# Performance work log

Hardware: AMD Instinct MI355X
Metric: run time of the kernel (lower is better)

The kernel has to match this reference:

```python
import jax, jax.numpy as jnp
import numpy as np

B, S, H, Q = 32, 128, 128, 3  # users, seq_len, hidden_size, quadkey_level
L = Q - 1  # number of mixing scales


def setup_inputs() -> dict:
    key = jax.random.key(0)
    ks = jax.random.split(key, 12)
    trend0 = jax.random.normal(ks[0], (B, S, H), dtype=jnp.float32)
    trend1 = jax.random.normal(ks[1], (B, S, H), dtype=jnp.float32)
    trend2 = jax.random.normal(ks[2], (B, S, H), dtype=jnp.float32)
    # Per-position prefix linears padded into dense tensors, zero-masked beyond
    # the prefix length j+1 so the ragged math is exact:
    #   W1[j, :j+1, :j+1] ~ Linear(j+1, j+1), b1[j, :j+1]
    #   W2[j, :j+1]      ~ Linear(j+1, 1),   b2[j]
    idx = jnp.arange(S)
    pm = (idx[None, :] <= idx[:, None]).astype(jnp.float32)  # [j, s]: s <= j
    W1 = jax.random.normal(ks[3], (L, S, S, S), dtype=jnp.float32) * 0.05
    W1 = W1 * pm[None, :, :, None] * pm[None, :, None, :]
    b1 = jax.random.normal(ks[4], (L, S, S), dtype=jnp.float32) * 0.05 * pm[None]
    W2 = jax.random.normal(ks[5], (L, S, S), dtype=jnp.float32) * 0.05 * pm[None]
    b2 = jax.random.normal(ks[6], (L, S), dtype=jnp.float32) * 0.05
    # shared output MLP: Linear(H,H)->GELU->Linear(H,H); stored as [in, out]
    Wm1 = jax.random.normal(ks[7], (H, H), dtype=jnp.float32) * 0.05
    bm1 = jax.random.normal(ks[8], (H,), dtype=jnp.float32) * 0.05
    Wm2 = jax.random.normal(ks[9], (H, H), dtype=jnp.float32) * 0.05
    bm2 = jax.random.normal(ks[10], (H,), dtype=jnp.float32) * 0.05
    return {"trend0": trend0, "trend1": trend1, "trend2": trend2,
            "W1": W1, "b1": b1, "W2": W2, "b2": b2,
            "Wm1": Wm1, "bm1": bm1, "Wm2": Wm2, "bm2": bm2}


def reference(trend0, trend1, trend2, W1, b1, W2, b2, Wm1, bm1, Wm2, bm2):
    gelu = lambda x: jax.nn.gelu(x, approximate=False)  # torch nn.GELU default
    mlp = lambda x: gelu(x @ Wm1 + bm1) @ Wm2 + bm2

    rev = [trend2, trend1, trend0]  # trend_list reversed
    out_low = rev[0]
    out_high = rev[1]
    outs = [out_low]
    for i in range(Q - 1):
        # vectorized ragged prefix mix: per position j, out_low[:, :j+1] (as [B,H,j+1])
        # -> Linear(j+1,j+1) -> GELU -> Linear(j+1,1). Zero-padding in W1/b1/W2
        # kills all contributions beyond the prefix (GELU(0)=0).
        y1 = jnp.einsum('bsh,jst->bhjt', out_low, W1[i]) + b1[i]  # [B,H,S,S]
        res = jnp.einsum('bhjt,jt->bjh', gelu(y1), W2[i]) + b2[i][None, :, None]
        out_high = out_high + res
        out_low = out_high
        if i + 2 <= Q - 1:
            out_high = rev[i + 2]
        out_low = mlp(out_low)
        outs.append(out_low)
    outs.reverse()
    return tuple(outs)
```

## Files before the change

kernel.cpp:

```cpp
#include <hip/hip_runtime.h>
#include <stdint.h>

#define BSH (32 * 128 * 128)

typedef __attribute__((ext_vector_type(8))) __bf16 bf16x8;
typedef __attribute__((ext_vector_type(4))) float f32x4;

__device__ __forceinline__ unsigned short f2bf(float f) {
  union { float f; unsigned u; } v; v.f = f;
  return (unsigned short)((v.u + 0x7FFFu + ((v.u >> 16) & 1u)) >> 16);
}

__device__ __forceinline__ float fast_exp2(float x) {
#if __has_builtin(__builtin_amdgcn_exp2f)
  return __builtin_amdgcn_exp2f(x);
#else
  float r; asm("v_exp_f32 %0, %1" : "=v"(r) : "v"(x)); return r;
#endif
}
__device__ __forceinline__ float fast_rcp(float x) {
#if __has_builtin(__builtin_amdgcn_rcpf)
  return __builtin_amdgcn_rcpf(x);
#else
  float r; asm("v_rcp_f32 %0, %1" : "=v"(r) : "v"(x)); return r;
#endif
}

__device__ __forceinline__ float gelu_f(float y) {
  float u = y * y;
  float p = __builtin_fmaf(u, 0.044715f, 1.0f) * y;
  float w = fast_exp2(p * 2.30220787f);
  return y - y * fast_rcp(1.0f + w);
}

__device__ __forceinline__ void transpose_block_c(const float* __restrict__ src,
                                                  unsigned short* __restrict__ dst,
                                                  unsigned short* lds) {
  const int tid = threadIdx.x;
  const float4* s4 = (const float4*)(src);
#pragma unroll
  for (int it = 0; it < 16; ++it) {
    int i4 = tid + it * 256;
    float4 v = s4[i4];
    int s = i4 >> 5;
    int t0 = (i4 * 4) & 127;
    unsigned short* pp = lds + s * 136 + t0;
    pp[0] = f2bf(v.x); pp[1] = f2bf(v.y); pp[2] = f2bf(v.z); pp[3] = f2bf(v.w);
  }
  __syncthreads();
#pragma unroll
  for (int it = 0; it < 8; ++it) {
    int c = tid + it * 256;
    int sc = c >> 7, tr = c & 127;
    unsigned short tmp[8] __attribute__((aligned(16)));
#pragma unroll
    for (int e = 0; e < 8; ++e) tmp[e] = lds[(sc * 8 + e) * 136 + tr];
    *(uint4*)(dst + (sc * 128 + tr) * 8) = *(const uint4*)tmp;
  }
}

__global__ __launch_bounds__(256) void prepass_kernel(
    const float* __restrict__ W1, const float* __restrict__ trend2,
    const float* __restrict__ Wm1, const float* __restrict__ Wm2,
    unsigned short* __restrict__ W1Tc, unsigned short* __restrict__ T2c,
    unsigned short* __restrict__ Wm1c, unsigned short* __restrict__ Wm2c,
    float* __restrict__ out2) {
  __shared__ unsigned short lds[128 * 136];
  const int bid = blockIdx.x;
  if (bid < 256) {
    int x = bid & 7, i = bid >> 3;
    int stage = i >> 4, u = i & 15;
    int m = u & 7, half = u >> 3;
    int jpp = x + 8 * m;
    int j = half ? 127 - jpp : jpp;
    int blk = stage * 128 + j;
    transpose_block_c(W1 + blk * 16384, W1Tc + blk * 16384, lds);
  } else if (bid < 288) {
    const int b = bid - 256;
    transpose_block_c(trend2 + b * 16384, T2c + b * 16384, lds);
    const float4* s4 = (const float4*)(trend2 + b * 16384);
    float4* d4 = (float4*)(out2 + b * 16384);
#pragma unroll
    for (int it = 0; it < 16; ++it)
      d4[threadIdx.x + it * 256] = s4[threadIdx.x + it * 256];
  } else if (bid == 288) {
    transpose_block_c(Wm1, Wm1c, lds);
  } else {
    transpose_block_c(Wm2, Wm2c, lds);
  }
}

__global__ __launch_bounds__(256, 3) void mix_mlp_kernel(
    const unsigned short* __restrict__ XTc,
    const unsigned short* __restrict__ W1Tj,
    const float* __restrict__ b1j,
    const float* __restrict__ W2j,
    const float* __restrict__ b2j,
    const float* __restrict__ trendR,
    const unsigned short* __restrict__ Wm1c,
    const unsigned short* __restrict__ Wm2c,
    const float* __restrict__ bm1,
    const float* __restrict__ bm2,
    float* __restrict__ outA,
    unsigned short* __restrict__ outTc) {
  __shared__ float res[512];
  __shared__ __align__(16) float xrow[2][128];
  __shared__ __align__(16) unsigned short urow[2][128];
  const int bid = blockIdx.x;
  const int b = bid >> 6;
  const int jp = bid & 63;
  const int js = jp, jb = 127 - jp;
  const int tid = threadIdx.x;
  const int wave = tid >> 6;
  const int p = wave & 1;
  const int mh = wave >> 1;
  const int lane = tid & 63;
  const int lane15 = lane & 15;
  const int quad = lane >> 4;

  const int nt_s = (js >> 4) + 1, ks_s = (js >> 5) + 1;
  const int nt_b = (jb >> 4) + 1, ks_b = (jb >> 5) + 1;

  const unsigned short* Bp = XTc + b * 16384 + (p * 64 + lane15) * 8;
  const unsigned short* As = W1Tj + js * 16384 + lane15 * 8;
  const unsigned short* Ab = W1Tj + jb * 16384 + lane15 * 8;
  const float C = -2.45546937f;

  bf16x8 Bv[4][4];
#pragma unroll
  for (int ks = 0; ks < 4; ++ks)
    if (ks < ks_b) {
      const int ko = (ks * 4 + quad) * 1024;
      Bv[ks][0] = *(const bf16x8*)(Bp + ko);
      Bv[ks][1] = *(const bf16x8*)(Bp + ko + 128);
      Bv[ks][2] = *(const bf16x8*)(Bp + ko + 256);
      Bv[ks][3] = *(const bf16x8*)(Bp + ko + 384);
    }

  float psum[2][4];
#pragma unroll
  for (int jj = 0; jj < 2; ++jj)
#pragma unroll
    for (int ni = 0; ni < 4; ++ni) psum[jj][ni] = 0.f;

  for (int mt = mh; mt < nt_b; mt += 2) {
    f32x4 acc[4];
#pragma unroll
    for (int ni = 0; ni < 4; ++ni) { f32x4 z = {0.f, 0.f, 0.f, 0.f}; acc[ni] = z; }
    const int mo = mt * 128;
#pragma unroll
    for (int ks = 0; ks < 4; ++ks)
      if (ks < ks_b) {
        bf16x8 a = *(const bf16x8*)(Ab + (ks * 4 + quad) * 1024 + mo);
        acc[0] = __builtin_amdgcn_mfma_f32_16x16x32_bf16(a, Bv[ks][0], acc[0], 0, 0, 0);
        acc[1] = __builtin_amdgcn_mfma_f32_16x16x32_bf16(a, Bv[ks][1], acc[1], 0, 0, 0);
        acc[2] = __builtin_amdgcn_mfma_f32_16x16x32_bf16(a, Bv[ks][2], acc[2], 0, 0, 0);
        acc[3] = __builtin_amdgcn_mfma_f32_16x16x32_bf16(a, Bv[ks][3], acc[3], 0, 0, 0);
      }
    const int tb = mt * 16 + quad * 4;
    float4 b1v = *(const float4*)(b1j + jb * 128 + tb);
    float4 w2v = *(const float4*)(W2j + jb * 128 + tb);
#pragma unroll
    for (int r = 0; r < 4; ++r) {
      float b1r = ((const float*)&b1v)[r];
      float w2r = ((const float*)&w2v)[r];
      float cb = C * b1r;
      float bw = b1r * w2r;
#pragma unroll
      for (int ni = 0; ni < 4; ++ni) {
        float a = acc[ni][r];
        float m = __builtin_fmaf(a, C, cb);
        float e = fast_exp2(m);
        float rr2 = fast_rcp(1.0f + e);
        float yw = __builtin_fmaf(a, w2r, bw);
        psum[1][ni] = __builtin_fmaf(yw, rr2, psum[1][ni]);
      }
    }
  }

  for (int mt = mh; mt < nt_s; mt += 2) {
    f32x4 acc[4];
#pragma unroll
    for (int ni = 0; ni < 4; ++ni) { f32x4 z = {0.f, 0.f, 0.f, 0.f}; acc[ni] = z; }
    const int mo = mt * 128;
#pragma unroll
    for (int ks = 0; ks < 2; ++ks)
      if (ks < ks_s) {
        bf16x8 a = *(const bf16x8*)(As + (ks * 4 + quad) * 1024 + mo);
        acc[0] = __builtin_amdgcn_mfma_f32_16x16x32_bf16(a, Bv[ks][0], acc[0], 0, 0, 0);
        acc[1] = __builtin_amdgcn_mfma_f32_16x16x32_bf16(a, Bv[ks][1], acc[1], 0, 0, 0);
        acc[2] = __builtin_amdgcn_mfma_f32_16x16x32_bf16(a, Bv[ks][2], acc[2], 0, 0, 0);
        acc[3] = __builtin_amdgcn_mfma_f32_16x16x32_bf16(a, Bv[ks][3], acc[3], 0, 0, 0);
      }
    const int tb = mt * 16 + quad * 4;
    float4 b1v = *(const float4*)(b1j + js * 128 + tb);
    float4 w2v = *(const float4*)(W2j + js * 128 + tb);
#pragma unroll
    for (int r = 0; r < 4; ++r) {
      float b1r = ((const float*)&b1v)[r];
      float w2r = ((const float*)&w2v)[r];
      float cb = C * b1r;
      float bw = b1r * w2r;
#pragma unroll
      for (int ni = 0; ni < 4; ++ni) {
        float a = acc[ni][r];
        float m = __builtin_fmaf(a, C, cb);
        float e = fast_exp2(m);
        float rr2 = fast_rcp(1.0f + e);
        float yw = __builtin_fmaf(a, w2r, bw);
        psum[0][ni] = __builtin_fmaf(yw, rr2, psum[0][ni]);
      }
    }
  }

#pragma unroll
  for (int jj = 0; jj < 2; ++jj)
#pragma unroll
    for (int ni = 0; ni < 4; ++ni) {
      float v = psum[jj][ni];
      v += __shfl_xor(v, 16, 64);
      v += __shfl_xor(v, 32, 64);
      psum[jj][ni] = v;
    }

  if (quad == 0) {
#pragma unroll
    for (int jj = 0; jj < 2; ++jj)
#pragma unroll
      for (int ni = 0; ni < 4; ++ni)
        res[wave * 128 + jj * 64 + ni * 16 + lane15] = psum[jj][ni];
  }
  __syncthreads();
  {
    const int l = tid & 15;
    const int nni = (tid >> 4) & 3;
    const int jj = (tid >> 6) & 1;
    const int pp = tid >> 7;
    const int j = jj ? jb : js;
    const int h = pp * 64 + nni * 16 + l;
    float v = res[tid] + res[tid + 256] + b2j[j] +
              trendR[(b * 128 + j) * 128 + h];
    xrow[jj][h] = v;
  }
  __syncthreads();

  const int arow = lane15 & 1;
  bf16x8 af[4];
#pragma unroll
  for (int ks = 0; ks < 4; ++ks) {
    const f32x4* xp = (const f32x4*)&xrow[arow][(ks * 4 + quad) * 8];
    f32x4 v0 = xp[0], v1 = xp[1];
    unsigned short t[8] __attribute__((aligned(16)));
    t[0] = f2bf(v0[0]); t[1] = f2bf(v0[1]); t[2] = f2bf(v0[2]); t[3] = f2bf(v0[3]);
    t[4] = f2bf(v1[0]); t[5] = f2bf(v1[1]); t[6] = f2bf(v1[2]); t[7] = f2bf(v1[3]);
    af[ks] = *(const bf16x8*)t;
  }
  f32x4 acc1[2];
  { f32x4 z = {0.f, 0.f, 0.f, 0.f}; acc1[0] = z; acc1[1] = z; }
#pragma unroll
  for (int ks = 0; ks < 4; ++ks) {
    int kq = ks * 4 + quad;
    bf16x8 w0 = *(const bf16x8*)(Wm1c + (kq * 128 + wave * 32 + lane15) * 8);
    bf16x8 w1 = *(const bf16x8*)(Wm1c + (kq * 128 + wave * 32 + 16 + lane15) * 8);
    acc1[0] = __builtin_amdgcn_mfma_f32_16x16x32_bf16(af[ks], w0, acc1[0], 0, 0, 0);
    acc1[1] = __builtin_amdgcn_mfma_f32_16x16x32_bf16(af[ks], w1, acc1[1], 0, 0, 0);
  }
  if (quad == 0) {
#pragma unroll
    for (int ni2 = 0; ni2 < 2; ++ni2) {
      int n = wave * 32 + ni2 * 16 + lane15;
      float bv = bm1[n];
      urow[0][n] = f2bf(gelu_f(acc1[ni2][0] + bv));
      urow[1][n] = f2bf(gelu_f(acc1[ni2][1] + bv));
    }
  }
  __syncthreads();
  bf16x8 uf[4];
#pragma unroll
  for (int ks = 0; ks < 4; ++ks)
    uf[ks] = *(const bf16x8*)&urow[arow][(ks * 4 + quad) * 8];
  f32x4 acc2[2];
  { f32x4 z = {0.f, 0.f, 0.f, 0.f}; acc2[0] = z; acc2[1] = z; }
#pragma unroll
  for (int ks = 0; ks < 4; ++ks) {
    int kq = ks * 4 + quad;
    bf16x8 w0 = *(const bf16x8*)(Wm2c + (kq * 128 + wave * 32 + lane15) * 8);
    bf16x8 w1 = *(const bf16x8*)(Wm2c + (kq * 128 + wave * 32 + 16 + lane15) * 8);
    acc2[0] = __builtin_amdgcn_mfma_f32_16x16x32_bf16(uf[ks], w0, acc2[0], 0, 0, 0);
    acc2[1] = __builtin_amdgcn_mfma_f32_16x16x32_bf16(uf[ks], w1, acc2[1], 0, 0, 0);
  }
  if (quad == 0) {
#pragma unroll
    for (int ni2 = 0; ni2 < 2; ++ni2) {
      int n = wave * 32 + ni2 * 16 + lane15;
      float bv = bm2[n];
#pragma unroll
      for (int r = 0; r < 2; ++r) {
        int j = r ? jb : js;
        float v = acc2[ni2][r] + bv;
        outA[(b * 128 + j) * 128 + n] = v;
        if (outTc)
          outTc[b * 16384 + ((j >> 3) * 128 + n) * 8 + (j & 7)] = f2bf(v);
      }
    }
  }
}

extern "C" void kernel_launch(void* const* d_in, const int* in_sizes, int n_in,
                              void* d_out, int out_size, void* d_ws, size_t ws_size,
                              hipStream_t stream) {
  (void)in_sizes; (void)n_in; (void)out_size; (void)ws_size;
  const float* trend0 = (const float*)d_in[0];
  const float* trend1 = (const float*)d_in[1];
  const float* trend2 = (const float*)d_in[2];
  const float* W1  = (const float*)d_in[3];
  const float* b1  = (const float*)d_in[4];
  const float* W2  = (const float*)d_in[5];
  const float* b2  = (const float*)d_in[6];
  const float* Wm1 = (const float*)d_in[7];
  const float* bm1 = (const float*)d_in[8];
  const float* Wm2 = (const float*)d_in[9];
  const float* bm2 = (const float*)d_in[10];
  float* out = (float*)d_out;
  char* ws = (char*)d_ws;

  unsigned short* W1Tc = (unsigned short*)(ws);
  unsigned short* T2c  = (unsigned short*)(ws + 8388608);
  unsigned short* A1Tc = (unsigned short*)(ws + 9437184);
  unsigned short* Wm1c = (unsigned short*)(ws + 10485760);
  unsigned short* Wm2c = (unsigned short*)(ws + 10518528);

  prepass_kernel<<<290, 256, 0, stream>>>(W1, trend2, Wm1, Wm2,
                                          W1Tc, T2c, Wm1c, Wm2c, out + 2 * BSH);
  mix_mlp_kernel<<<2048, 256, 0, stream>>>(T2c, W1Tc, b1, W2, b2, trend1,
                                           Wm1c, Wm2c, bm1, bm2,
                                           out + BSH, A1Tc);
  mix_mlp_kernel<<<2048, 256, 0, stream>>>(A1Tc, W1Tc + 128 * 16384, b1 + 16384,
                                           W2 + 16384, b2 + 128, trend0,
                                           Wm1c, Wm2c, bm1, bm2,
                                           out, (unsigned short*)nullptr);
}
```

Measured before the change: 140.6 us.

## Split prepass transposes into quarter blocks and batch A-fragment loads before MFMAs

The prepass now splits each 128x128 transpose into four 32-row parts handled by separate blocks, giving 1154 blocks with a smaller LDS tile instead of 290. This raises parallelism and occupancy for the memory-bound conversion, and LDS stores are widened to 8-byte writes. In the mix kernel the ks-bound guards are removed, so all K slices are always loaded and multiplied, and all A fragments are loaded before the MFMA chain to expose more memory-level parallelism. Dropping the guards adds redundant MFMAs on zero-padded regions for small prefixes but removes branching.

```diff
diff --git a/kernel.cpp b/kernel.cpp
--- a/kernel.cpp
+++ b/kernel.cpp
@@ -33,29 +33,31 @@
   return y - y * fast_rcp(1.0f + w);
 }
 
-__device__ __forceinline__ void transpose_block_c(const float* __restrict__ src,
-                                                  unsigned short* __restrict__ dst,
-                                                  unsigned short* lds) {
+__device__ __forceinline__ void transpose_part(const float* __restrict__ src,
+                                               unsigned short* __restrict__ dst,
+                                               unsigned short* lds, int part) {
   const int tid = threadIdx.x;
-  const float4* s4 = (const float4*)(src);
-#pragma unroll
-  for (int it = 0; it < 16; ++it) {
+  const float4* s4 = (const float4*)(src) + part * 1024;
+  __syncthreads();
+#pragma unroll
+  for (int it = 0; it < 4; ++it) {
     int i4 = tid + it * 256;
     float4 v = s4[i4];
     int s = i4 >> 5;
     int t0 = (i4 * 4) & 127;
-    unsigned short* pp = lds + s * 136 + t0;
-    pp[0] = f2bf(v.x); pp[1] = f2bf(v.y); pp[2] = f2bf(v.z); pp[3] = f2bf(v.w);
-  }
-  __syncthreads();
-#pragma unroll
-  for (int it = 0; it < 8; ++it) {
+    unsigned short t[4] __attribute__((aligned(8)));
+    t[0] = f2bf(v.x); t[1] = f2bf(v.y); t[2] = f2bf(v.z); t[3] = f2bf(v.w);
+    *(uint2*)(lds + s * 136 + t0) = *(const uint2*)t;
+  }
+  __syncthreads();
+#pragma unroll
+  for (int it = 0; it < 2; ++it) {
     int c = tid + it * 256;
-    int sc = c >> 7, tr = c & 127;
+    int kql = c >> 7, tr = c & 127;
     unsigned short tmp[8] __attribute__((aligned(16)));
 #pragma unroll
-    for (int e = 0; e < 8; ++e) tmp[e] = lds[(sc * 8 + e) * 136 + tr];
-    *(uint4*)(dst + (sc * 128 + tr) * 8) = *(const uint4*)tmp;
+    for (int e = 0; e < 8; ++e) tmp[e] = lds[(kql * 8 + e) * 136 + tr];
+    *(uint4*)(dst + ((part * 4 + kql) * 128 + tr) * 8) = *(const uint4*)tmp;
   }
 }
 
@@ -65,28 +67,36 @@
     unsigned short* __restrict__ W1Tc, unsigned short* __restrict__ T2c,
     unsigned short* __restrict__ Wm1c, unsigned short* __restrict__ Wm2c,
     float* __restrict__ out2) {
-  __shared__ unsigned short lds[128 * 136];
+  __shared__ __align__(16) unsigned short lds[32 * 136];
   const int bid = blockIdx.x;
-  if (bid < 256) {
-    int x = bid & 7, i = bid >> 3;
+  if (bid < 1024) {
+    int part = bid >> 8, w = bid & 255;
+    int x = w & 7, i = w >> 3;
     int stage = i >> 4, u = i & 15;
     int m = u & 7, half = u >> 3;
     int jpp = x + 8 * m;
     int j = half ? 127 - jpp : jpp;
     int blk = stage * 128 + j;
-    transpose_block_c(W1 + blk * 16384, W1Tc + blk * 16384, lds);
-  } else if (bid < 288) {
-    const int b = bid - 256;
-    transpose_block_c(trend2 + b * 16384, T2c + b * 16384, lds);
+    transpose_part(W1 + blk * 16384, W1Tc + blk * 16384, lds, part);
+  } else if (bid < 1152) {
+    int t = bid - 1024;
+    int part = t >> 5, b = t & 31;
+    transpose_part(trend2 + b * 16384, T2c + b * 16384, lds, part);
     const float4* s4 = (const float4*)(trend2 + b * 16384);
     float4* d4 = (float4*)(out2 + b * 16384);
 #pragma unroll
-    for (int it = 0; it < 16; ++it)
-      d4[threadIdx.x + it * 256] = s4[threadIdx.x + it * 256];
-  } else if (bid == 288) {
-    transpose_block_c(Wm1, Wm1c, lds);
+    for (int it = 0; it < 4; ++it) {
+      int i = part * 1024 + threadIdx.x + it * 256;
+      d4[i] = s4[i];
+    }
+  } else if (bid == 1152) {
+#pragma unroll
+    for (int part = 0; part < 4; ++part)
+      transpose_part(Wm1, Wm1c, lds, part);
   } else {
-    transpose_block_c(Wm2, Wm2c, lds);
+#pragma unroll
+    for (int part = 0; part < 4; ++part)
+      transpose_part(Wm2, Wm2c, lds, part);
   }
 }
 
@@ -118,8 +128,8 @@
   const int lane15 = lane & 15;
   const int quad = lane >> 4;
 
-  const int nt_s = (js >> 4) + 1, ks_s = (js >> 5) + 1;
-  const int nt_b = (jb >> 4) + 1, ks_b = (jb >> 5) + 1;
+  const int nt_s = (js >> 4) + 1;
+  const int nt_b = (jb >> 4) + 1;
 
   const unsigned short* Bp = XTc + b * 16384 + (p * 64 + lane15) * 8;
   const unsigned short* As = W1Tj + js * 16384 + lane15 * 8;
@@ -128,14 +138,13 @@
 
   bf16x8 Bv[4][4];
 #pragma unroll
-  for (int ks = 0; ks < 4; ++ks)
-    if (ks < ks_b) {
-      const int ko = (ks * 4 + quad) * 1024;
-      Bv[ks][0] = *(const bf16x8*)(Bp + ko);
-      Bv[ks][1] = *(const bf16x8*)(Bp + ko + 128);
-      Bv[ks][2] = *(const bf16x8*)(Bp + ko + 256);
-      Bv[ks][3] = *(const bf16x8*)(Bp + ko + 384);
-    }
+  for (int ks = 0; ks < 4; ++ks) {
+    const int ko = (ks * 4 + quad) * 1024;
+    Bv[ks][0] = *(const bf16x8*)(Bp + ko);
+    Bv[ks][1] = *(const bf16x8*)(Bp + ko + 128);
+    Bv[ks][2] = *(const bf16x8*)(Bp + ko + 256);
+    Bv[ks][3] = *(const bf16x8*)(Bp + ko + 384);
+  }
 
   float psum[2][4];
 #pragma unroll
@@ -144,22 +153,24 @@
     for (int ni = 0; ni < 4; ++ni) psum[jj][ni] = 0.f;
 
   for (int mt = mh; mt < nt_b; mt += 2) {
-    f32x4 acc[4];
-#pragma unroll
-    for (int ni = 0; ni < 4; ++ni) { f32x4 z = {0.f, 0.f, 0.f, 0.f}; acc[ni] = z; }
     const int mo = mt * 128;
+    bf16x8 a[4];
 #pragma unroll
     for (int ks = 0; ks < 4; ++ks)
-      if (ks < ks_b) {
-        bf16x8 a = *(const bf16x8*)(Ab + (ks * 4 + quad) * 1024 + mo);
-        acc[0] = __builtin_amdgcn_mfma_f32_16x16x32_bf16(a, Bv[ks][0], acc[0], 0, 0, 0);
-        acc[1] = __builtin_amdgcn_mfma_f32_16x16x32_bf16(a, Bv[ks][1], acc[1], 0, 0, 0);
-        acc[2] = __builtin_amdgcn_mfma_f32_16x16x32_bf16(a, Bv[ks][2], acc[2], 0, 0, 0);
-        acc[3] = __builtin_amdgcn_mfma_f32_16x16x32_bf16(a, Bv[ks][3], acc[3], 0, 0, 0);
-      }
+      a[ks] = *(const bf16x8*)(Ab + (ks * 4 + quad) * 1024 + mo);
     const int tb = mt * 16 + quad * 4;
     float4 b1v = *(const float4*)(b1j + jb * 128 + tb);
     float4 w2v = *(const float4*)(W2j + jb * 128 + tb);
+    f32x4 acc[4];
+#pragma unroll
+    for (int ni = 0; ni < 4; ++ni) { f32x4 z = {0.f, 0.f, 0.f, 0.f}; acc[ni] = z; }
+#pragma unroll
+    for (int ks = 0; ks < 4; ++ks) {
+      acc[0] = __builtin_amdgcn_mfma_f32_16x16x32_bf16(a[ks], Bv[ks][0], acc[0], 0, 0, 0);
+      acc[1] = __builtin_amdgcn_mfma_f32_16x16x32_bf16(a[ks], Bv[ks][1], acc[1], 0, 0, 0);
+      acc[2] = __builtin_amdgcn_mfma_f32_16x16x32_bf16(a[ks], Bv[ks][2], acc[2], 0, 0, 0);
+      acc[3] = __builtin_amdgcn_mfma_f32_16x16x32_bf16(a[ks], Bv[ks][3], acc[3], 0, 0, 0);
+    }
 #pragma unroll
     for (int r = 0; r < 4; ++r) {
       float b1r = ((const float*)&b1v)[r];
@@ -168,33 +179,35 @@
       float bw = b1r * w2r;
 #pragma unroll
       for (int ni = 0; ni < 4; ++ni) {
-        float a = acc[ni][r];
-        float m = __builtin_fmaf(a, C, cb);
+        float av = acc[ni][r];
+        float m = __builtin_fmaf(av, C, cb);
         float e = fast_exp2(m);
         float rr2 = fast_rcp(1.0f + e);
-        float yw = __builtin_fmaf(a, w2r, bw);
+        float yw = __builtin_fmaf(av, w2r, bw);
         psum[1][ni] = __builtin_fmaf(yw, rr2, psum[1][ni]);
       }
     }
   }
 
   for (int mt = mh; mt < nt_s; mt += 2) {
-    f32x4 acc[4];
-#pragma unroll
-    for (int ni = 0; ni < 4; ++ni) { f32x4 z = {0.f, 0.f, 0.f, 0.f}; acc[ni] = z; }
     const int mo = mt * 128;
+    bf16x8 a[2];
 #pragma unroll
     for (int ks = 0; ks < 2; ++ks)
-      if (ks < ks_s) {
-        bf16x8 a = *(const bf16x8*)(As + (ks * 4 + quad) * 1024 + mo);
-        acc[0] = __builtin_amdgcn_mfma_f32_16x16x32_bf16(a, Bv[ks][0], acc[0], 0, 0, 0);
-        acc[1] = __builtin_amdgcn_mfma_f32_16x16x32_bf16(a, Bv[ks][1], acc[1], 0, 0, 0);
-        acc[2] = __builtin_amdgcn_mfma_f32_16x16x32_bf16(a, Bv[ks][2], acc[2], 0, 0, 0);
-        acc[3] = __builtin_amdgcn_mfma_f32_16x16x32_bf16(a, Bv[ks][3], acc[3], 0, 0, 0);
-      }
+      a[ks] = *(const bf16x8*)(As + (ks * 4 + quad) * 1024 + mo);
     const int tb = mt * 16 + quad * 4;
     float4 b1v = *(const float4*)(b1j + js * 128 + tb);
     float4 w2v = *(const float4*)(W2j + js * 128 + tb);
+    f32x4 acc[4];
+#pragma unroll
+    for (int ni = 0; ni < 4; ++ni) { f32x4 z = {0.f, 0.f, 0.f, 0.f}; acc[ni] = z; }
+#pragma unroll
+    for (int ks = 0; ks < 2; ++ks) {
+      acc[0] = __builtin_amdgcn_mfma_f32_16x16x32_bf16(a[ks], Bv[ks][0], acc[0], 0, 0, 0);
+      acc[1] = __builtin_amdgcn_mfma_f32_16x16x32_bf16(a[ks], Bv[ks][1], acc[1], 0, 0, 0);
+      acc[2] = __builtin_amdgcn_mfma_f32_16x16x32_bf16(a[ks], Bv[ks][2], acc[2], 0, 0, 0);
+      acc[3] = __builtin_amdgcn_mfma_f32_16x16x32_bf16(a[ks], Bv[ks][3], acc[3], 0, 0, 0);
+    }
 #pragma unroll
     for (int r = 0; r < 4; ++r) {
       float b1r = ((const float*)&b1v)[r];
@@ -203,11 +216,11 @@
       float bw = b1r * w2r;
 #pragma unroll
       for (int ni = 0; ni < 4; ++ni) {
-        float a = acc[ni][r];
-        float m = __builtin_fmaf(a, C, cb);
+        float av = acc[ni][r];
+        float m = __builtin_fmaf(av, C, cb);
         float e = fast_exp2(m);
         float rr2 = fast_rcp(1.0f + e);
-        float yw = __builtin_fmaf(a, w2r, bw);
+        float yw = __builtin_fmaf(av, w2r, bw);
         psum[0][ni] = __builtin_fmaf(yw, rr2, psum[0][ni]);
       }
     }
@@ -330,8 +343,8 @@
   unsigned short* Wm1c = (unsigned short*)(ws + 10485760);
   unsigned short* Wm2c = (unsigned short*)(ws + 10518528);
 
-  prepass_kernel<<<290, 256, 0, stream>>>(W1, trend2, Wm1, Wm2,
-                                          W1Tc, T2c, Wm1c, Wm2c, out + 2 * BSH);
+  prepass_kernel<<<1154, 256, 0, stream>>>(W1, trend2, Wm1, Wm2,
+                                           W1Tc, T2c, Wm1c, Wm2c, out + 2 * BSH);
   mix_mlp_kernel<<<2048, 256, 0, stream>>>(T2c, W1Tc, b1, W2, b2, trend1,
                                            Wm1c, Wm2c, bm1, bm2,
                                            out + BSH, A1Tc);
```

Result: no change. 139.9 us (-0.5%).
